# Kernel tuning notes

Measured on AMD Instinct MI355X. Metric: run time of the kernel, lower is better.

The kernel has to match this reference:

```python
import jax, jax.numpy as jnp
import numpy as np

D_MODEL = 1024
NUM_HEADS = 16
D_K = D_MODEL // NUM_HEADS
B, S = 2, 2048


def setup_inputs() -> dict:
    key = jax.random.key(0)
    ks = jax.random.split(key, 9)
    scale = 1.0 / np.sqrt(D_MODEL)
    return {
        "hidden_states": jax.random.normal(ks[0], (B, S, D_MODEL), dtype=jnp.float32),
        "attention_mask": jnp.ones((B, S, S), dtype=jnp.int32),
        "Wq": jax.random.normal(ks[1], (D_MODEL, D_MODEL), dtype=jnp.float32) * scale,
        "bq": jnp.zeros((D_MODEL,), dtype=jnp.float32),
        "Wk": jax.random.normal(ks[2], (D_MODEL, D_MODEL), dtype=jnp.float32) * scale,
        "bk": jnp.zeros((D_MODEL,), dtype=jnp.float32),
        "Wv": jax.random.normal(ks[3], (D_MODEL, D_MODEL), dtype=jnp.float32) * scale,
        "bv": jnp.zeros((D_MODEL,), dtype=jnp.float32),
        "Wo": jax.random.normal(ks[4], (D_MODEL, D_MODEL), dtype=jnp.float32) * scale,
        "bo": jnp.zeros((D_MODEL,), dtype=jnp.float32),
    }


def reference(hidden_states, attention_mask, Wq, bq, Wk, bk, Wv, bv, Wo, bo):
    b, s, _ = hidden_states.shape
    # torch Linear: y = x @ W.T + b
    def proj(W, bias):
        y = jnp.einsum('bsd,ed->bse', hidden_states, W) + bias
        return y.reshape(b, s, NUM_HEADS, D_K).transpose(0, 2, 1, 3)  # [B,H,S,dk]
    q = proj(Wq, bq)
    k = proj(Wk, bk)
    v = proj(Wv, bv)
    scores = jnp.einsum('bnqd,bnkd->bnqk', q, k) / np.sqrt(D_K)
    mask = attention_mask[:, None, :, :]  # [B,1,S,S]
    scores = jnp.where(mask == 0, jnp.float32(-1e9), scores)
    attn = jax.nn.softmax(scores, axis=-1)  # dropout = identity (eval)
    ctx = jnp.einsum('bnqk,bnkd->bnqd', attn, v)
    ctx = ctx.transpose(0, 2, 1, 3).reshape(b, s, D_MODEL)
    return jnp.einsum('bsd,ed->bse', ctx, Wo) + bo
```

## Files before the change

kernel.cpp:

```cpp
#include <hip/hip_runtime.h>

typedef short short8 __attribute__((ext_vector_type(8)));
typedef float floatx4 __attribute__((ext_vector_type(4)));
typedef float floatx16 __attribute__((ext_vector_type(16)));
typedef unsigned short ushort4v __attribute__((ext_vector_type(4)));

#define DEV static __device__ __forceinline__

DEV unsigned short f2bf(float f) {
  unsigned int u = __builtin_bit_cast(unsigned int, f);
  u += 0x7fffu + ((u >> 16) & 1u);
  return (unsigned short)(u >> 16);
}

DEV unsigned int pkbf2(float a, float b) {
  unsigned int ua = __builtin_bit_cast(unsigned int, a) + 0x8000u;
  unsigned int ub = __builtin_bit_cast(unsigned int, b) + 0x8000u;
  return (ua >> 16) | (ub & 0xffff0000u);
}

DEV void gload16(const unsigned short* g, unsigned short* l) {
  __builtin_amdgcn_global_load_lds((__attribute__((address_space(1))) void*)g,
                                   (__attribute__((address_space(3))) void*)l,
                                   16, 0, 0);
}

__global__ void prep_kernel(const float* __restrict__ hs, const float* __restrict__ Wq,
                            const float* __restrict__ Wk, const float* __restrict__ Wv,
                            const float* __restrict__ Wo, const int* __restrict__ mask,
                            unsigned short* __restrict__ xbf, unsigned short* __restrict__ wqkv,
                            unsigned short* __restrict__ wobf,
                            unsigned long long* __restrict__ bits) {
  const int bid = blockIdx.x;
  if (bid < 8192) {
    size_t i4 = ((size_t)bid * 256 + threadIdx.x) * 4;
    const float* src;
    unsigned short* dst;
    if (i4 < 4194304) {
      src = hs + i4; dst = xbf + i4;
    } else if (i4 < 7340032) {
      size_t o = i4 - 4194304;
      size_t lo = o & 1048575;
      src = (o < 1048576) ? (Wq + lo) : ((o < 2097152) ? (Wk + lo) : (Wv + lo));
      dst = wqkv + o;
    } else {
      size_t o = i4 - 7340032;
      src = Wo + o; dst = wobf + o;
    }
    float4 v = *(const float4*)src;
    ushort4v u;
    u.x = f2bf(v.x); u.y = f2bf(v.y); u.z = f2bf(v.z); u.w = f2bf(v.w);
    *(ushort4v*)dst = u;
  } else {
    int w = (bid - 8192) * 256 + threadIdx.x;
    const int4* p = (const int4*)(mask + (size_t)w * 64);
    unsigned long long r = 0ull;
#pragma unroll
    for (int j = 0; j < 16; ++j) {
      int4 m = p[j];
      r |= (unsigned long long)(m.x != 0) << (j * 4 + 0);
      r |= (unsigned long long)(m.y != 0) << (j * 4 + 1);
      r |= (unsigned long long)(m.z != 0) << (j * 4 + 2);
      r |= (unsigned long long)(m.w != 0) << (j * 4 + 3);
    }
    bits[w] = r;
  }
}

__global__ void __launch_bounds__(256) qkv_gemm(
    const unsigned short* __restrict__ X, const unsigned short* __restrict__ W,
    const float* __restrict__ bq, const float* __restrict__ bk, const float* __restrict__ bv,
    unsigned short* __restrict__ Qb, unsigned short* __restrict__ Kb,
    unsigned short* __restrict__ Vt) {
  __shared__ __align__(16) unsigned short As[128 * 32];
  __shared__ __align__(16) unsigned short Bs[128 * 32];
  const int tid = threadIdx.x;
  const int lane = tid & 63, wv = tid >> 6;
  const int wm = wv >> 1, wn = wv & 1;
  const int quad = lane >> 4, l15 = lane & 15;
  const int mb = blockIdx.y, nb = blockIdx.x;
  const bool sw = (nb < 16);

  const unsigned short* ga = X + (size_t)(mb * 128 + (tid >> 2)) * 1024 + (tid & 3) * 8;
  const unsigned short* gb = W + (size_t)(nb * 128 + (tid >> 2)) * 1024 + (tid & 3) * 8;
  unsigned short* la1 = As + tid * 8;
  unsigned short* la2 = As + 2048 + tid * 8;
  unsigned short* lb1 = Bs + tid * 8;
  unsigned short* lb2 = Bs + 2048 + tid * 8;

  const int wx = sw ? wn : wm;
  const int ww = sw ? wm : wn;

  floatx4 acc[4][4] = {};
  for (int kt = 0; kt < 32; ++kt) {
    const int k0 = kt * 32;
    gload16(ga + k0, la1);
    gload16(ga + k0 + 65536, la2);
    gload16(gb + k0, lb1);
    gload16(gb + k0 + 65536, lb2);
    __syncthreads();
    short8 xa[4], wb[4];
#pragma unroll
    for (int i = 0; i < 4; ++i) {
      xa[i] = *(const short8*)&As[(wx * 64 + i * 16 + l15) * 32 + quad * 8];
      wb[i] = *(const short8*)&Bs[(ww * 64 + i * 16 + l15) * 32 + quad * 8];
    }
    if (sw) {
#pragma unroll
      for (int mt = 0; mt < 4; ++mt)
#pragma unroll
        for (int nt = 0; nt < 4; ++nt)
          acc[mt][nt] = __builtin_amdgcn_mfma_f32_16x16x32_bf16(wb[mt], xa[nt], acc[mt][nt], 0, 0, 0);
    } else {
#pragma unroll
      for (int mt = 0; mt < 4; ++mt)
#pragma unroll
        for (int nt = 0; nt < 4; ++nt)
          acc[mt][nt] = __builtin_amdgcn_mfma_f32_16x16x32_bf16(xa[mt], wb[nt], acc[mt][nt], 0, 0, 0);
    }
    __syncthreads();
  }

  if (sw) {
#pragma unroll
    for (int mt = 0; mt < 4; ++mt) {
      const int wc0 = nb * 128 + wm * 64 + mt * 16 + quad * 4;
      const int mat = wc0 >> 10;
      const int nl0 = wc0 & 1023;
      const int hh = nl0 >> 6, d0 = nl0 & 63;
      const float4 b4 = *(const float4*)((mat ? bk : bq) + nl0);
      const float scl = mat ? 1.0f : 0.180336879f;
      unsigned short* dst = mat ? Kb : Qb;
#pragma unroll
      for (int nt = 0; nt < 4; ++nt) {
        const int colx = mb * 128 + wn * 64 + nt * 16 + l15;
        const int bb = colx >> 11, s = colx & 2047;
        ushort4v pv;
        pv[0] = f2bf((acc[mt][nt][0] + b4.x) * scl);
        pv[1] = f2bf((acc[mt][nt][1] + b4.y) * scl);
        pv[2] = f2bf((acc[mt][nt][2] + b4.z) * scl);
        pv[3] = f2bf((acc[mt][nt][3] + b4.w) * scl);
        *(ushort4v*)&dst[((size_t)(bb * 16 + hh) * 2048 + s) * 64 + d0] = pv;
      }
    }
  } else {
#pragma unroll
    for (int nt = 0; nt < 4; ++nt) {
      const int col = nb * 128 + wn * 64 + nt * 16 + l15;
      const int nl = col & 1023;
      const float bias = bv[nl];
      const int hh = nl >> 6, d = nl & 63;
#pragma unroll
      for (int mt = 0; mt < 4; ++mt) {
        const int row0 = mb * 128 + wm * 64 + mt * 16 + quad * 4;
        const int bb = row0 >> 11, s = row0 & 2047;
        ushort4v pv;
#pragma unroll
        for (int r = 0; r < 4; ++r) pv[r] = f2bf(acc[mt][nt][r] + bias);
        *(ushort4v*)&Vt[((size_t)(bb * 16 + hh) * 64 + d) * 2048 + s] = pv;
      }
    }
  }
}

__global__ void __launch_bounds__(256, 2) attn_kernel(
    const unsigned short* __restrict__ Qb, const unsigned short* __restrict__ Kb,
    const unsigned short* __restrict__ Vt, const unsigned long long* __restrict__ mbits,
    unsigned short* __restrict__ ctx) {
  __shared__ __align__(16) unsigned short Ks[2][128 * 64];
  __shared__ __align__(16) unsigned short Vs[2][64 * 128];
  const int tid = threadIdx.x;
  const int lane = tid & 63, wv = tid >> 6;
  const int l31 = lane & 31, h = lane >> 5;
  const int pair = blockIdx.x >> 4, qt = blockIdx.x & 15;
  const int b_ = pair >> 4, hd = pair & 15;
  const int qg = qt * 128 + wv * 32 + l31;
  const size_t pbase = (size_t)pair * (2048 * 64);

  int kofs[4], vofs[4];
  const unsigned short* kgp[4];
  const unsigned short* vgp[4];
#pragma unroll
  for (int it = 0; it < 4; ++it) {
    const int ch = it * 256 + tid;
    const int kr = ch >> 3, kc = ch & 7;
    kofs[it] = kr * 64 + ((kc ^ (kr & 7)) * 8);
    kgp[it] = Kb + pbase + (size_t)kr * 64 + kc * 8;
    const int vr = ch >> 4, vc = ch & 15;
    vofs[it] = vr * 128 + ((vc ^ ((vr & 7) << 1)) * 8);
    vgp[it] = Vt + pbase + (size_t)vr * 2048 + vc * 8;
  }

  short8 qf[4];
#pragma unroll
  for (int ks = 0; ks < 4; ++ks)
    qf[ks] = *(const short8*)(Qb + pbase + (size_t)qg * 64 + ks * 16 + h * 8);

  union { unsigned short u[8]; short8 s8; } one_u;
#pragma unroll
  for (int i = 0; i < 8; ++i) one_u.u[i] = 0x3F80;
  const short8 ones = one_u.s8;

  floatx16 NCv;
#pragma unroll
  for (int r = 0; r < 16; ++r) NCv[r] = -10.0f;

  floatx16 acc_o[2] = {};
  floatx16 acc_sum = {};

  short8 kr8[4], vr8[4];
#pragma unroll
  for (int it = 0; it < 4; ++it) {
    kr8[it] = *(const short8*)kgp[it];
    vr8[it] = *(const short8*)vgp[it];
  }

  for (int kb16 = 0; kb16 < 16; ++kb16) {
    unsigned short* ksb = Ks[kb16 & 1];
    unsigned short* vsb = Vs[kb16 & 1];
#pragma unroll
    for (int it = 0; it < 4; ++it) {
      *(short8*)&ksb[kofs[it]] = kr8[it];
      *(short8*)&vsb[vofs[it]] = vr8[it];
    }
    __syncthreads();
    if (kb16 < 15) {
      const size_t ko = (size_t)(kb16 + 1) * 8192;
      const size_t vo = (size_t)(kb16 + 1) * 128;
#pragma unroll
      for (int it = 0; it < 4; ++it) {
        kr8[it] = *(const short8*)(kgp[it] + ko);
        vr8[it] = *(const short8*)(vgp[it] + vo);
      }
    }

    const unsigned long long* mrow = mbits + ((size_t)b_ * 2048 + qg) * 32 + kb16 * 2;
    const unsigned long long w0 = mrow[0], w1 = mrow[1];
    const bool anymask = __any((w0 & w1) != ~0ull);

#pragma unroll
    for (int kb = 0; kb < 4; ++kb) {
      floatx16 accs;
      {
        const int krow = kb * 32 + l31;
        short8 kf = *(const short8*)&ksb[krow * 64 + ((h ^ (krow & 7)) * 8)];
        accs = __builtin_amdgcn_mfma_f32_32x32x16_bf16(kf, qf[0], NCv, 0, 0, 0);
#pragma unroll
        for (int ks = 1; ks < 4; ++ks) {
          short8 kf2 = *(const short8*)&ksb[krow * 64 + (((ks * 2 + h) ^ (krow & 7)) * 8)];
          accs = __builtin_amdgcn_mfma_f32_32x32x16_bf16(kf2, qf[ks], accs, 0, 0, 0);
        }
      }
      if (anymask) {
        const unsigned long long w = (kb < 2) ? w0 : w1;
#pragma unroll
        for (int reg = 0; reg < 16; ++reg) {
          const int kl = (reg & 3) + 8 * (reg >> 2) + 4 * h;
          const int bit = (kb & 1) * 32 + kl;
          if (!((w >> bit) & 1ull)) accs[reg] = -1e9f;
        }
      }
      unsigned int pk[8];
#pragma unroll
      for (int i = 0; i < 8; ++i)
        pk[i] = pkbf2(exp2f(accs[2 * i]), exp2f(accs[2 * i + 1]));

#pragma unroll
      for (int u = 0; u < 2; ++u) {
        const unsigned int own0 = h ? pk[4 * u + 2] : pk[4 * u + 0];
        const unsigned int own1 = h ? pk[4 * u + 3] : pk[4 * u + 1];
        const unsigned int snd0 = h ? pk[4 * u + 0] : pk[4 * u + 2];
        const unsigned int snd1 = h ? pk[4 * u + 1] : pk[4 * u + 3];
        const unsigned int t0 = __shfl_xor(snd0, 32);
        const unsigned int t1 = __shfl_xor(snd1, 32);
        union { unsigned int w[4]; short8 s8; } af;
        af.w[0] = h ? t0 : own0;
        af.w[1] = h ? t1 : own1;
        af.w[2] = h ? own0 : t0;
        af.w[3] = h ? own1 : t1;
        const int t = kb * 2 + u;
#pragma unroll
        for (int nt = 0; nt < 2; ++nt) {
          const int vrow = nt * 32 + l31;
          short8 vf = *(const short8*)&vsb[vrow * 128 + (((t * 2 + h) ^ ((vrow & 7) << 1)) * 8)];
          acc_o[nt] = __builtin_amdgcn_mfma_f32_32x32x16_bf16(af.s8, vf, acc_o[nt], 0, 0, 0);
        }
        acc_sum = __builtin_amdgcn_mfma_f32_32x32x16_bf16(af.s8, ones, acc_sum, 0, 0, 0);
      }
    }
  }

#pragma unroll
  for (int reg = 0; reg < 16; ++reg) {
    const float s = acc_sum[reg];
    const float rinv = (s > 0.f) ? 1.f / s : 1.f;
    const int ql = (reg & 3) + 8 * (reg >> 2) + 4 * h;
    const size_t base = ((size_t)b_ * 2048 + qt * 128 + wv * 32 + ql) * 1024 + hd * 64;
    ctx[base + l31]      = f2bf(acc_o[0][reg] * rinv);
    ctx[base + 32 + l31] = f2bf(acc_o[1][reg] * rinv);
  }
}

__global__ void __launch_bounds__(256) out_gemm(
    const unsigned short* __restrict__ C, const unsigned short* __restrict__ W,
    const float* __restrict__ bo, float* __restrict__ out) {
  __shared__ __align__(16) unsigned short As[128 * 32];
  __shared__ __align__(16) unsigned short Bs[128 * 32];
  const int tid = threadIdx.x;
  const int lane = tid & 63, wv = tid >> 6;
  const int wm = wv >> 1, wn = wv & 1;
  const int quad = lane >> 4, l15 = lane & 15;
  const int mb = blockIdx.y, nb = blockIdx.x;

  const unsigned short* ga = C + (size_t)(mb * 128 + (tid >> 2)) * 1024 + (tid & 3) * 8;
  const unsigned short* gb = W + (size_t)(nb * 128 + (tid >> 2)) * 1024 + (tid & 3) * 8;
  unsigned short* la1 = As + tid * 8;
  unsigned short* la2 = As + 2048 + tid * 8;
  unsigned short* lb1 = Bs + tid * 8;
  unsigned short* lb2 = Bs + 2048 + tid * 8;

  floatx4 acc[4][4] = {};
  for (int kt = 0; kt < 32; ++kt) {
    const int k0 = kt * 32;
    gload16(ga + k0, la1);
    gload16(ga + k0 + 65536, la2);
    gload16(gb + k0, lb1);
    gload16(gb + k0 + 65536, lb2);
    __syncthreads();
    short8 af[4], bfr[4];
#pragma unroll
    for (int i = 0; i < 4; ++i) {
      af[i]  = *(const short8*)&As[(wm * 64 + i * 16 + l15) * 32 + quad * 8];
      bfr[i] = *(const short8*)&Bs[(wn * 64 + i * 16 + l15) * 32 + quad * 8];
    }
#pragma unroll
    for (int mt = 0; mt < 4; ++mt)
#pragma unroll
      for (int nt = 0; nt < 4; ++nt)
        acc[mt][nt] = __builtin_amdgcn_mfma_f32_16x16x32_bf16(af[mt], bfr[nt], acc[mt][nt], 0, 0, 0);
    __syncthreads();
  }
#pragma unroll
  for (int nt = 0; nt < 4; ++nt) {
    const int col = nb * 128 + wn * 64 + nt * 16 + l15;
    const float bias = bo[col];
#pragma unroll
    for (int mt = 0; mt < 4; ++mt)
#pragma unroll
      for (int r = 0; r < 4; ++r) {
        const int row = mb * 128 + wm * 64 + mt * 16 + quad * 4 + r;
        out[(size_t)row * 1024 + col] = acc[mt][nt][r] + bias;
      }
  }
}

extern "C" void kernel_launch(void* const* d_in, const int* in_sizes, int n_in,
                              void* d_out, int out_size, void* d_ws, size_t ws_size,
                              hipStream_t stream) {
  const float* hs = (const float*)d_in[0];
  const int* mask = (const int*)d_in[1];
  const float* Wq = (const float*)d_in[2];
  const float* bq = (const float*)d_in[3];
  const float* Wk = (const float*)d_in[4];
  const float* bk = (const float*)d_in[5];
  const float* Wv = (const float*)d_in[6];
  const float* bv = (const float*)d_in[7];
  const float* Wo = (const float*)d_in[8];
  const float* bo = (const float*)d_in[9];
  float* out = (float*)d_out;

  char* ws = (char*)d_ws;
  unsigned short* xbf  = (unsigned short*)(ws + 0);
  unsigned short* wqkv = (unsigned short*)(ws + 8388608);
  unsigned short* wobf = (unsigned short*)(ws + 14680064);
  unsigned short* Qb   = (unsigned short*)(ws + 16777216);
  unsigned short* Kb   = (unsigned short*)(ws + 25165824);
  unsigned short* Vt   = (unsigned short*)(ws + 33554432);
  unsigned short* ctx  = (unsigned short*)(ws + 41943040);
  unsigned long long* mbits = (unsigned long long*)(ws + 50331648);

  prep_kernel<<<8704, 256, 0, stream>>>(hs, Wq, Wk, Wv, Wo, mask, xbf, wqkv, wobf, mbits);
  qkv_gemm<<<dim3(24, 32), 256, 0, stream>>>(xbf, wqkv, bq, bk, bv, Qb, Kb, Vt);
  attn_kernel<<<512, 256, 0, stream>>>(Qb, Kb, Vt, mbits, ctx);
  out_gemm<<<dim3(8, 32), 256, 0, stream>>>(ctx, wobf, bo, out);
}
```

Measured before the change: 278.5 us.

## Halve GEMM and attention tiles for more blocks, use direct LDS loads in attention

The QKV and output GEMMs now use 64-row M tiles instead of 128. This doubles their grid size and halves accumulator registers, with a launch bound of 2 blocks per SIMD. The attention kernel moves to 128-thread blocks covering 64 queries, which doubles the grid to 1024 blocks. It also replaces the register-staged double-buffered K/V prefetch with single-buffered global_load_lds copies, using a source-side XOR swizzle and a barrier after each tile. The goal is better CU occupancy and load balance on the many-CU GPU. The cost is lost K/V prefetch overlap and K/V being streamed twice as often per query head.

```diff
diff --git a/kernel.cpp b/kernel.cpp
--- a/kernel.cpp
+++ b/kernel.cpp
@@ -67,53 +67,56 @@
   }
 }
 
-__global__ void __launch_bounds__(256) qkv_gemm(
+__global__ void __launch_bounds__(256, 2) qkv_gemm(
     const unsigned short* __restrict__ X, const unsigned short* __restrict__ W,
     const float* __restrict__ bq, const float* __restrict__ bk, const float* __restrict__ bv,
     unsigned short* __restrict__ Qb, unsigned short* __restrict__ Kb,
     unsigned short* __restrict__ Vt) {
-  __shared__ __align__(16) unsigned short As[128 * 32];
+  __shared__ __align__(16) unsigned short As[64 * 32];
   __shared__ __align__(16) unsigned short Bs[128 * 32];
   const int tid = threadIdx.x;
   const int lane = tid & 63, wv = tid >> 6;
-  const int wm = wv >> 1, wn = wv & 1;
   const int quad = lane >> 4, l15 = lane & 15;
   const int mb = blockIdx.y, nb = blockIdx.x;
   const bool sw = (nb < 16);
 
-  const unsigned short* ga = X + (size_t)(mb * 128 + (tid >> 2)) * 1024 + (tid & 3) * 8;
+  const unsigned short* ga = X + (size_t)(mb * 64 + (tid >> 2)) * 1024 + (tid & 3) * 8;
   const unsigned short* gb = W + (size_t)(nb * 128 + (tid >> 2)) * 1024 + (tid & 3) * 8;
   unsigned short* la1 = As + tid * 8;
-  unsigned short* la2 = As + 2048 + tid * 8;
   unsigned short* lb1 = Bs + tid * 8;
   unsigned short* lb2 = Bs + 2048 + tid * 8;
 
-  const int wx = sw ? wn : wm;
-  const int ww = sw ? wm : wn;
-
-  floatx4 acc[4][4] = {};
+  floatx4 acc[2][4] = {};
   for (int kt = 0; kt < 32; ++kt) {
     const int k0 = kt * 32;
     gload16(ga + k0, la1);
-    gload16(ga + k0 + 65536, la2);
     gload16(gb + k0, lb1);
     gload16(gb + k0 + 65536, lb2);
     __syncthreads();
-    short8 xa[4], wb[4];
-#pragma unroll
-    for (int i = 0; i < 4; ++i) {
-      xa[i] = *(const short8*)&As[(wx * 64 + i * 16 + l15) * 32 + quad * 8];
-      wb[i] = *(const short8*)&Bs[(ww * 64 + i * 16 + l15) * 32 + quad * 8];
-    }
     if (sw) {
-#pragma unroll
-      for (int mt = 0; mt < 4; ++mt)
+      short8 wb[2], xa[4];
+#pragma unroll
+      for (int i = 0; i < 2; ++i)
+        wb[i] = *(const short8*)&Bs[(wv * 32 + i * 16 + l15) * 32 + quad * 8];
+#pragma unroll
+      for (int i = 0; i < 4; ++i)
+        xa[i] = *(const short8*)&As[(i * 16 + l15) * 32 + quad * 8];
+#pragma unroll
+      for (int mt = 0; mt < 2; ++mt)
 #pragma unroll
         for (int nt = 0; nt < 4; ++nt)
           acc[mt][nt] = __builtin_amdgcn_mfma_f32_16x16x32_bf16(wb[mt], xa[nt], acc[mt][nt], 0, 0, 0);
     } else {
-#pragma unroll
-      for (int mt = 0; mt < 4; ++mt)
+      const int wm = wv >> 1, wn = wv & 1;
+      short8 xa[2], wb[4];
+#pragma unroll
+      for (int i = 0; i < 2; ++i)
+        xa[i] = *(const short8*)&As[(wm * 32 + i * 16 + l15) * 32 + quad * 8];
+#pragma unroll
+      for (int i = 0; i < 4; ++i)
+        wb[i] = *(const short8*)&Bs[(wn * 64 + i * 16 + l15) * 32 + quad * 8];
+#pragma unroll
+      for (int mt = 0; mt < 2; ++mt)
 #pragma unroll
         for (int nt = 0; nt < 4; ++nt)
           acc[mt][nt] = __builtin_amdgcn_mfma_f32_16x16x32_bf16(xa[mt], wb[nt], acc[mt][nt], 0, 0, 0);
@@ -123,8 +126,8 @@
 
   if (sw) {
 #pragma unroll
-    for (int mt = 0; mt < 4; ++mt) {
-      const int wc0 = nb * 128 + wm * 64 + mt * 16 + quad * 4;
+    for (int mt = 0; mt < 2; ++mt) {
+      const int wc0 = nb * 128 + wv * 32 + mt * 16 + quad * 4;
       const int mat = wc0 >> 10;
       const int nl0 = wc0 & 1023;
       const int hh = nl0 >> 6, d0 = nl0 & 63;
@@ -133,7 +136,7 @@
       unsigned short* dst = mat ? Kb : Qb;
 #pragma unroll
       for (int nt = 0; nt < 4; ++nt) {
-        const int colx = mb * 128 + wn * 64 + nt * 16 + l15;
+        const int colx = mb * 64 + nt * 16 + l15;
         const int bb = colx >> 11, s = colx & 2047;
         ushort4v pv;
         pv[0] = f2bf((acc[mt][nt][0] + b4.x) * scl);
@@ -144,6 +147,7 @@
       }
     }
   } else {
+    const int wm = wv >> 1, wn = wv & 1;
 #pragma unroll
     for (int nt = 0; nt < 4; ++nt) {
       const int col = nb * 128 + wn * 64 + nt * 16 + l15;
@@ -151,8 +155,8 @@
       const float bias = bv[nl];
       const int hh = nl >> 6, d = nl & 63;
 #pragma unroll
-      for (int mt = 0; mt < 4; ++mt) {
-        const int row0 = mb * 128 + wm * 64 + mt * 16 + quad * 4;
+      for (int mt = 0; mt < 2; ++mt) {
+        const int row0 = mb * 64 + wm * 32 + mt * 16 + quad * 4;
         const int bb = row0 >> 11, s = row0 & 2047;
         ushort4v pv;
 #pragma unroll
@@ -163,33 +167,26 @@
   }
 }
 
-__global__ void __launch_bounds__(256, 2) attn_kernel(
+__global__ void __launch_bounds__(128, 2) attn_kernel(
     const unsigned short* __restrict__ Qb, const unsigned short* __restrict__ Kb,
     const unsigned short* __restrict__ Vt, const unsigned long long* __restrict__ mbits,
     unsigned short* __restrict__ ctx) {
-  __shared__ __align__(16) unsigned short Ks[2][128 * 64];
-  __shared__ __align__(16) unsigned short Vs[2][64 * 128];
+  __shared__ __align__(16) unsigned short Ks[128 * 64];
+  __shared__ __align__(16) unsigned short Vs[64 * 128];
   const int tid = threadIdx.x;
   const int lane = tid & 63, wv = tid >> 6;
   const int l31 = lane & 31, h = lane >> 5;
-  const int pair = blockIdx.x >> 4, qt = blockIdx.x & 15;
+  const int pair = blockIdx.x >> 5, qt = blockIdx.x & 31;
   const int b_ = pair >> 4, hd = pair & 15;
-  const int qg = qt * 128 + wv * 32 + l31;
+  const int qg = qt * 64 + wv * 32 + l31;
   const size_t pbase = (size_t)pair * (2048 * 64);
 
-  int kofs[4], vofs[4];
-  const unsigned short* kgp[4];
-  const unsigned short* vgp[4];
-#pragma unroll
-  for (int it = 0; it < 4; ++it) {
-    const int ch = it * 256 + tid;
-    const int kr = ch >> 3, kc = ch & 7;
-    kofs[it] = kr * 64 + ((kc ^ (kr & 7)) * 8);
-    kgp[it] = Kb + pbase + (size_t)kr * 64 + kc * 8;
-    const int vr = ch >> 4, vc = ch & 15;
-    vofs[it] = vr * 128 + ((vc ^ ((vr & 7) << 1)) * 8);
-    vgp[it] = Vt + pbase + (size_t)vr * 2048 + vc * 8;
-  }
+  const int krl = lane >> 3;
+  const unsigned short* pkK = Kb + pbase + (size_t)(wv * 8 + krl) * 64 +
+                              (((lane & 7) ^ (krl & 7)) * 8);
+  const int vrl = wv * 4 + (lane >> 4);
+  const unsigned short* pkV = Vt + pbase + (size_t)vrl * 2048 +
+                              (((lane & 15) ^ ((vrl & 7) << 1)) * 8);
 
   short8 qf[4];
 #pragma unroll
@@ -208,31 +205,14 @@
   floatx16 acc_o[2] = {};
   floatx16 acc_sum = {};
 
-  short8 kr8[4], vr8[4];
-#pragma unroll
-  for (int it = 0; it < 4; ++it) {
-    kr8[it] = *(const short8*)kgp[it];
-    vr8[it] = *(const short8*)vgp[it];
-  }
-
   for (int kb16 = 0; kb16 < 16; ++kb16) {
-    unsigned short* ksb = Ks[kb16 & 1];
-    unsigned short* vsb = Vs[kb16 & 1];
-#pragma unroll
-    for (int it = 0; it < 4; ++it) {
-      *(short8*)&ksb[kofs[it]] = kr8[it];
-      *(short8*)&vsb[vofs[it]] = vr8[it];
-    }
-    __syncthreads();
-    if (kb16 < 15) {
-      const size_t ko = (size_t)(kb16 + 1) * 8192;
-      const size_t vo = (size_t)(kb16 + 1) * 128;
-#pragma unroll
-      for (int it = 0; it < 4; ++it) {
-        kr8[it] = *(const short8*)(kgp[it] + ko);
-        vr8[it] = *(const short8*)(vgp[it] + vo);
-      }
-    }
+#pragma unroll
+    for (int g = 0; g < 8; ++g)
+      gload16(pkK + (size_t)kb16 * 8192 + g * 1024, Ks + (g * 128 + wv * 64) * 8);
+#pragma unroll
+    for (int g = 0; g < 8; ++g)
+      gload16(pkV + (size_t)kb16 * 128 + g * 16384, Vs + (g * 128 + wv * 64) * 8);
+    __syncthreads();
 
     const unsigned long long* mrow = mbits + ((size_t)b_ * 2048 + qg) * 32 + kb16 * 2;
     const unsigned long long w0 = mrow[0], w1 = mrow[1];
@@ -243,11 +223,11 @@
       floatx16 accs;
       {
         const int krow = kb * 32 + l31;
-        short8 kf = *(const short8*)&ksb[krow * 64 + ((h ^ (krow & 7)) * 8)];
+        short8 kf = *(const short8*)&Ks[krow * 64 + ((h ^ (krow & 7)) * 8)];
         accs = __builtin_amdgcn_mfma_f32_32x32x16_bf16(kf, qf[0], NCv, 0, 0, 0);
 #pragma unroll
         for (int ks = 1; ks < 4; ++ks) {
-          short8 kf2 = *(const short8*)&ksb[krow * 64 + (((ks * 2 + h) ^ (krow & 7)) * 8)];
+          short8 kf2 = *(const short8*)&Ks[krow * 64 + (((ks * 2 + h) ^ (krow & 7)) * 8)];
           accs = __builtin_amdgcn_mfma_f32_32x32x16_bf16(kf2, qf[ks], accs, 0, 0, 0);
         }
       }
@@ -282,12 +262,13 @@
 #pragma unroll
         for (int nt = 0; nt < 2; ++nt) {
           const int vrow = nt * 32 + l31;
-          short8 vf = *(const short8*)&vsb[vrow * 128 + (((t * 2 + h) ^ ((vrow & 7) << 1)) * 8)];
+          short8 vf = *(const short8*)&Vs[vrow * 128 + (((t * 2 + h) ^ ((vrow & 7) << 1)) * 8)];
           acc_o[nt] = __builtin_amdgcn_mfma_f32_32x32x16_bf16(af.s8, vf, acc_o[nt], 0, 0, 0);
         }
         acc_sum = __builtin_amdgcn_mfma_f32_32x32x16_bf16(af.s8, ones, acc_sum, 0, 0, 0);
       }
     }
+    __syncthreads();
   }
 
 #pragma unroll
@@ -295,16 +276,16 @@
     const float s = acc_sum[reg];
     const float rinv = (s > 0.f) ? 1.f / s : 1.f;
     const int ql = (reg & 3) + 8 * (reg >> 2) + 4 * h;
-    const size_t base = ((size_t)b_ * 2048 + qt * 128 + wv * 32 + ql) * 1024 + hd * 64;
+    const size_t base = ((size_t)b_ * 2048 + qt * 64 + wv * 32 + ql) * 1024 + hd * 64;
     ctx[base + l31]      = f2bf(acc_o[0][reg] * rinv);
     ctx[base + 32 + l31] = f2bf(acc_o[1][reg] * rinv);
   }
 }
 
-__global__ void __launch_bounds__(256) out_gemm(
+__global__ void __launch_bounds__(256, 2) out_gemm(
     const unsigned short* __restrict__ C, const unsigned short* __restrict__ W,
     const float* __restrict__ bo, float* __restrict__ out) {
-  __shared__ __align__(16) unsigned short As[128 * 32];
+  __shared__ __align__(16) unsigned short As[64 * 32];
   __shared__ __align__(16) unsigned short Bs[128 * 32];
   const int tid = threadIdx.x;
   const int lane = tid & 63, wv = tid >> 6;
@@ -312,29 +293,28 @@
   const int quad = lane >> 4, l15 = lane & 15;
   const int mb = blockIdx.y, nb = blockIdx.x;
 
-  const unsigned short* ga = C + (size_t)(mb * 128 + (tid >> 2)) * 1024 + (tid & 3) * 8;
+  const unsigned short* ga = C + (size_t)(mb * 64 + (tid >> 2)) * 1024 + (tid & 3) * 8;
   const unsigned short* gb = W + (size_t)(nb * 128 + (tid >> 2)) * 1024 + (tid & 3) * 8;
   unsigned short* la1 = As + tid * 8;
-  unsigned short* la2 = As + 2048 + tid * 8;
   unsigned short* lb1 = Bs + tid * 8;
   unsigned short* lb2 = Bs + 2048 + tid * 8;
 
-  floatx4 acc[4][4] = {};
+  floatx4 acc[2][4] = {};
   for (int kt = 0; kt < 32; ++kt) {
     const int k0 = kt * 32;
     gload16(ga + k0, la1);
-    gload16(ga + k0 + 65536, la2);
     gload16(gb + k0, lb1);
     gload16(gb + k0 + 65536, lb2);
     __syncthreads();
-    short8 af[4], bfr[4];
-#pragma unroll
-    for (int i = 0; i < 4; ++i) {
-      af[i]  = *(const short8*)&As[(wm * 64 + i * 16 + l15) * 32 + quad * 8];
+    short8 af[2], bfr[4];
+#pragma unroll
+    for (int i = 0; i < 2; ++i)
+      af[i] = *(const short8*)&As[(wm * 32 + i * 16 + l15) * 32 + quad * 8];
+#pragma unroll
+    for (int i = 0; i < 4; ++i)
       bfr[i] = *(const short8*)&Bs[(wn * 64 + i * 16 + l15) * 32 + quad * 8];
-    }
-#pragma unroll
-    for (int mt = 0; mt < 4; ++mt)
+#pragma unroll
+    for (int mt = 0; mt < 2; ++mt)
 #pragma unroll
       for (int nt = 0; nt < 4; ++nt)
         acc[mt][nt] = __builtin_amdgcn_mfma_f32_16x16x32_bf16(af[mt], bfr[nt], acc[mt][nt], 0, 0, 0);
@@ -345,10 +325,10 @@
     const int col = nb * 128 + wn * 64 + nt * 16 + l15;
     const float bias = bo[col];
 #pragma unroll
-    for (int mt = 0; mt < 4; ++mt)
+    for (int mt = 0; mt < 2; ++mt)
 #pragma unroll
       for (int r = 0; r < 4; ++r) {
-        const int row = mb * 128 + wm * 64 + mt * 16 + quad * 4 + r;
+        const int row = mb * 64 + wm * 32 + mt * 16 + quad * 4 + r;
         out[(size_t)row * 1024 + col] = acc[mt][nt][r] + bias;
       }
   }
@@ -380,7 +360,7 @@
   unsigned long long* mbits = (unsigned long long*)(ws + 50331648);
 
   prep_kernel<<<8704, 256, 0, stream>>>(hs, Wq, Wk, Wv, Wo, mask, xbf, wqkv, wobf, mbits);
-  qkv_gemm<<<dim3(24, 32), 256, 0, stream>>>(xbf, wqkv, bq, bk, bv, Qb, Kb, Vt);
-  attn_kernel<<<512, 256, 0, stream>>>(Qb, Kb, Vt, mbits, ctx);
-  out_gemm<<<dim3(8, 32), 256, 0, stream>>>(ctx, wobf, bo, out);
-}
+  qkv_gemm<<<dim3(24, 64), 256, 0, stream>>>(xbf, wqkv, bq, bk, bv, Qb, Kb, Vt);
+  attn_kernel<<<1024, 128, 0, stream>>>(Qb, Kb, Vt, mbits, ctx);
+  out_gemm<<<dim3(8, 64), 256, 0, stream>>>(ctx, wobf, bo, out);
+}
```

Result: no change. 273.5 us (-1.8%).

## Use direct global-to-LDS loads and smaller attention blocks with head-major ordering

Applied to the files above, without the earlier changes.

Rewrites the attention kernel's K/V staging to use global_load_lds async copies into double-buffered shared memory, with the swizzle applied on the global source side. This removes the register round-trip for K/V tiles. Blocks shrink to 128 threads covering 64 queries, launched as 1024 blocks with head-pair as the fast index, which doubles the block count for occupancy and improves K/V sharing across concurrent blocks. In exchange, each block re-reads the full K/V for fewer queries, doubling K/V global traffic, and a trailing barrier is added every iteration.

```diff
diff --git a/kernel.cpp b/kernel.cpp
--- a/kernel.cpp
+++ b/kernel.cpp
@@ -163,7 +163,7 @@
   }
 }
 
-__global__ void __launch_bounds__(256, 2) attn_kernel(
+__global__ void __launch_bounds__(128, 2) attn_kernel(
     const unsigned short* __restrict__ Qb, const unsigned short* __restrict__ Kb,
     const unsigned short* __restrict__ Vt, const unsigned long long* __restrict__ mbits,
     unsigned short* __restrict__ ctx) {
@@ -172,24 +172,17 @@
   const int tid = threadIdx.x;
   const int lane = tid & 63, wv = tid >> 6;
   const int l31 = lane & 31, h = lane >> 5;
-  const int pair = blockIdx.x >> 4, qt = blockIdx.x & 15;
+  const int pair = blockIdx.x & 31, qt = blockIdx.x >> 5;
   const int b_ = pair >> 4, hd = pair & 15;
-  const int qg = qt * 128 + wv * 32 + l31;
+  const int qg = qt * 64 + wv * 32 + l31;
   const size_t pbase = (size_t)pair * (2048 * 64);
 
-  int kofs[4], vofs[4];
-  const unsigned short* kgp[4];
-  const unsigned short* vgp[4];
-#pragma unroll
-  for (int it = 0; it < 4; ++it) {
-    const int ch = it * 256 + tid;
-    const int kr = ch >> 3, kc = ch & 7;
-    kofs[it] = kr * 64 + ((kc ^ (kr & 7)) * 8);
-    kgp[it] = Kb + pbase + (size_t)kr * 64 + kc * 8;
-    const int vr = ch >> 4, vc = ch & 15;
-    vofs[it] = vr * 128 + ((vc ^ ((vr & 7) << 1)) * 8);
-    vgp[it] = Vt + pbase + (size_t)vr * 2048 + vc * 8;
-  }
+  const int krl = lane >> 3;
+  const unsigned short* pkK = Kb + pbase + (size_t)(wv * 8 + krl) * 64 +
+                              (((lane & 7) ^ (krl & 7)) * 8);
+  const int vrl = wv * 4 + (lane >> 4);
+  const unsigned short* pkV = Vt + pbase + (size_t)vrl * 2048 +
+                              (((lane & 15) ^ ((vrl & 7) << 1)) * 8);
 
   short8 qf[4];
 #pragma unroll
@@ -208,30 +201,25 @@
   floatx16 acc_o[2] = {};
   floatx16 acc_sum = {};
 
-  short8 kr8[4], vr8[4];
-#pragma unroll
-  for (int it = 0; it < 4; ++it) {
-    kr8[it] = *(const short8*)kgp[it];
-    vr8[it] = *(const short8*)vgp[it];
-  }
+#pragma unroll
+  for (int g = 0; g < 8; ++g)
+    gload16(pkK + g * 1024, &Ks[0][(g * 128 + wv * 64) * 8]);
+#pragma unroll
+  for (int g = 0; g < 8; ++g)
+    gload16(pkV + g * 16384, &Vs[0][(g * 128 + wv * 64) * 8]);
+  __syncthreads();
 
   for (int kb16 = 0; kb16 < 16; ++kb16) {
-    unsigned short* ksb = Ks[kb16 & 1];
-    unsigned short* vsb = Vs[kb16 & 1];
-#pragma unroll
-    for (int it = 0; it < 4; ++it) {
-      *(short8*)&ksb[kofs[it]] = kr8[it];
-      *(short8*)&vsb[vofs[it]] = vr8[it];
-    }
-    __syncthreads();
+    const int cur = kb16 & 1;
+    const unsigned short* ksb = Ks[cur];
+    const unsigned short* vsb = Vs[cur];
     if (kb16 < 15) {
-      const size_t ko = (size_t)(kb16 + 1) * 8192;
-      const size_t vo = (size_t)(kb16 + 1) * 128;
-#pragma unroll
-      for (int it = 0; it < 4; ++it) {
-        kr8[it] = *(const short8*)(kgp[it] + ko);
-        vr8[it] = *(const short8*)(vgp[it] + vo);
-      }
+#pragma unroll
+      for (int g = 0; g < 8; ++g)
+        gload16(pkK + (size_t)(kb16 + 1) * 8192 + g * 1024, &Ks[cur ^ 1][(g * 128 + wv * 64) * 8]);
+#pragma unroll
+      for (int g = 0; g < 8; ++g)
+        gload16(pkV + (size_t)(kb16 + 1) * 128 + g * 16384, &Vs[cur ^ 1][(g * 128 + wv * 64) * 8]);
     }
 
     const unsigned long long* mrow = mbits + ((size_t)b_ * 2048 + qg) * 32 + kb16 * 2;
@@ -288,6 +276,7 @@
         acc_sum = __builtin_amdgcn_mfma_f32_32x32x16_bf16(af.s8, ones, acc_sum, 0, 0, 0);
       }
     }
+    __syncthreads();
   }
 
 #pragma unroll
@@ -295,7 +284,7 @@
     const float s = acc_sum[reg];
     const float rinv = (s > 0.f) ? 1.f / s : 1.f;
     const int ql = (reg & 3) + 8 * (reg >> 2) + 4 * h;
-    const size_t base = ((size_t)b_ * 2048 + qt * 128 + wv * 32 + ql) * 1024 + hd * 64;
+    const size_t base = ((size_t)b_ * 2048 + qt * 64 + wv * 32 + ql) * 1024 + hd * 64;
     ctx[base + l31]      = f2bf(acc_o[0][reg] * rinv);
     ctx[base + 32 + l31] = f2bf(acc_o[1][reg] * rinv);
   }
@@ -381,6 +370,6 @@
 
   prep_kernel<<<8704, 256, 0, stream>>>(hs, Wq, Wk, Wv, Wo, mask, xbf, wqkv, wobf, mbits);
   qkv_gemm<<<dim3(24, 32), 256, 0, stream>>>(xbf, wqkv, bq, bk, bv, Qb, Kb, Vt);
-  attn_kernel<<<512, 256, 0, stream>>>(Qb, Kb, Vt, mbits, ctx);
+  attn_kernel<<<1024, 128, 0, stream>>>(Qb, Kb, Vt, mbits, ctx);
   out_gemm<<<dim3(8, 32), 256, 0, stream>>>(ctx, wobf, bo, out);
 }
```

New measurement: 298.1 us. 1.07x slower.
